# Kernel tuning notes

Hardware: AMD Instinct MI355X
Metric: run time of the kernel (lower is better)

Reference implementation:

```python
import jax, jax.numpy as jnp
import numpy as np

N_DOF = 7
HIDDEN = 256
BATCH = 32768
L_DIAG_OFFSET = 1e-3
FRICTION_EPS = 100.0


def setup_inputs() -> dict:
    key = jax.random.key(0)
    ks = jax.random.split(key, 16)
    n, H, B = N_DOF, HIDDEN, BATCH
    ntril = n * (n - 1) // 2

    def xavier(k, shape):
        fan_out, fan_in = shape
        std = (2.0 / (fan_in + fan_out)) ** 0.5
        return jax.random.normal(k, shape, jnp.float32) * std

    return {
        "q":   jax.random.normal(ks[0], (B, n), jnp.float32),
        "qd":  jax.random.normal(ks[1], (B, n), jnp.float32),
        "qdd": jax.random.normal(ks[2], (B, n), jnp.float32),
        # MLP trunk (hidden_depth = 3)
        "W0": xavier(ks[3], (H, n)),  "b0": jnp.zeros((H,), jnp.float32),
        "W1": xavier(ks[4], (H, H)),  "b1": jnp.zeros((H,), jnp.float32),
        "W2": xavier(ks[5], (H, H)),  "b2": jnp.zeros((H,), jnp.float32),
        # heads: gravity g, Cholesky diagonal, Cholesky strict-lower
        "Wg":  xavier(ks[6], (n, H)),     "bg":  jnp.zeros((n,), jnp.float32),
        "Wld": xavier(ks[7], (n, H)),     "bld": jnp.zeros((n,), jnp.float32),
        "Wlt": xavier(ks[8], (ntril, H)), "blt": jnp.zeros((ntril,), jnp.float32),
        # friction model parameters (init 0.1 each)
        "fd": jnp.full((n,), 0.1, jnp.float32),
        "fc": jnp.full((n,), 0.1, jnp.float32),
        "fs": jnp.full((n,), 0.1, jnp.float32),
        "fv": jnp.full((n,), 0.1, jnp.float32),
    }


def reference(q, qd, qdd, W0, b0, W1, b1, W2, b2, Wg, bg, Wld, bld, Wlt, blt,
              fd, fc, fs, fv):
    n = N_DOF
    B = q.shape[0]
    sp = jax.nn.softplus

    def net(qq):  # qq: [n] single sample
        h = sp(W0 @ qq + b0)
        h = sp(W1 @ h + b1)
        h = sp(W2 @ h + b2)
        g = Wg @ h + bg                      # [n]
        Ld_raw = Wld @ h + bld               # [n]
        Ld = sp(Ld_raw)                      # softplus diag activation
        Lt = Wlt @ h + blt                   # [n_tril]
        return (Ld, Lt), (g, Ld, Lt, Ld_raw)

    # per-sample Jacobians of (L_diag, L_tril) wrt q (forward mode, n_dof tangents)
    (jLd, jLt), (g, Ld, Lt, Ld_raw) = jax.vmap(jax.jacfwd(net, has_aux=True))(q)
    # jLd: [B,n,n], jLt: [B,ntril,n]

    idx = np.arange(n)
    rows, cols = np.tril_indices(n, -1)

    L = (jnp.zeros((B, n, n), q.dtype)
         .at[:, idx, idx].set(Ld)
         .at[:, rows, cols].set(Lt)
         + L_DIAG_OFFSET * jnp.eye(n, dtype=q.dtype))          # [B,n,n]
    L_dq = (jnp.zeros((B, n, n, n), q.dtype)
            .at[:, idx, idx, :].set(jLd)
            .at[:, rows, cols, :].set(jLt))                    # [B,n,n,n] (last = dq)

    LT = jnp.swapaxes(L, 1, 2)
    L_dqT = jnp.swapaxes(L_dq, 1, 2)

    Hm = jnp.einsum('bij,bjk->bik', L, LT)                      # mass matrix
    L_dt = jnp.einsum('bijc,bc->bij', L_dq, qd)                 # dL/dt
    L_dtT = jnp.swapaxes(L_dt, 1, 2)
    H_dt = jnp.einsum('bij,bjk->bik', L, L_dtT) + jnp.einsum('bij,bjk->bik', L_dt, LT)
    H_dq = (jnp.einsum('bijc,bjk->bikc', L_dq, LT)
            + jnp.einsum('bij,bjkc->bikc', L, L_dqT))           # [B,n,n,n]
    H_dq_qd = jnp.einsum('bijc,bj->bic', H_dq, qd)
    qdT_H_dq_qd = jnp.einsum('bi,bic->bc', qd, H_dq_qd)
    c = jnp.einsum('bij,bj->bi', H_dt, qd) - 0.5 * qdT_H_dq_qd  # Coriolis

    fv_c = jnp.clip(fv, 1e-3, None)
    tau_fric = (fc + fs * jnp.exp(-qd ** 2 / fv_c)) * jnp.tanh(FRICTION_EPS * qd) + fd * qd

    tau_pred = jnp.einsum('bij,bj->bi', Hm, qdd) + c + g + tau_fric
    return (tau_pred, Hm, c, g, tau_fric, Ld_raw)
```

## Files before the change

### kernel.cpp

```cpp
#include <hip/hip_runtime.h>
#include <cmath>

#define NDOF 7
#define HID  256
#define SPW  8
#define NCOL 64
#define SWZ(c) (((c) & 15) << 3)

typedef __bf16 bf16x8 __attribute__((ext_vector_type(8)));
typedef float  f32x4  __attribute__((ext_vector_type(4)));

#define OFF_W2 65536
#define OFF_WH 131072
#define OFF_W0 143360
#define WS_TOT 151552

__device__ __forceinline__ float softplus_fast(float x){
    float e = __expf(-fabsf(x));
    return fmaxf(x, 0.0f) + __logf(1.0f + e);
}
__device__ __forceinline__ float sigmoid_fast(float x){
    float e  = __expf(-fabsf(x));
    float rc = 1.0f / (1.0f + e);
    return (x >= 0.0f) ? rc : e * rc;
}
__device__ __forceinline__ float tanh_fast(float y){
    float e2 = __expf(-2.0f * fabsf(y));
    float t  = (1.0f - e2) / (1.0f + e2);
    return (y >= 0.0f) ? t : -t;
}
__device__ __forceinline__ unsigned bf16bits(float x){
    union { float f; unsigned u; } v; v.f = x;
    unsigned lsb = (v.u >> 16) & 1;
    return ((v.u + 0x7fffu + lsb) >> 16) & 0xffffu;
}

__global__ void convert_weights(const float* __restrict__ W1, const float* __restrict__ W2,
                                const float* __restrict__ Wg, const float* __restrict__ Wld,
                                const float* __restrict__ Wlt, const float* __restrict__ W0,
                                __bf16* __restrict__ ws)
{
    int i = blockIdx.x * 256 + threadIdx.x;
    if (i < OFF_W2)        ws[i] = (__bf16)W1[i];
    else if (i < OFF_WH)   ws[i] = (__bf16)W2[i - OFF_W2];
    else if (i < OFF_W0) {
        int j = i - OFF_WH;
        int r = j >> 8, k = j & 255;
        float v = 0.0f;
        if (r < 7)       v = Wg [r * HID + k];
        else if (r < 14) v = Wld[(r - 7) * HID + k];
        else if (r < 35) v = Wlt[(r - 14) * HID + k];
        ws[i] = (__bf16)v;
    } else if (i < WS_TOT) {
        int j = i - OFF_W0;
        int r = j >> 5, k = j & 31;
        ws[i] = (__bf16)((k < 7) ? W0[r * 7 + k] : 0.0f);
    }
}

template<int KK>
__device__ __forceinline__ void mlp_layer(
    const __bf16* __restrict__ Wb, int astride, const float* __restrict__ bp,
    __bf16* Xs, int w, int lo, int hi, const int* srcl, bool prim)
{
    f32x4 acc[4][4];
    #pragma unroll
    for (int mi = 0; mi < 4; ++mi)
        #pragma unroll
        for (int ni = 0; ni < 4; ++ni) acc[mi][ni] = (f32x4){0.f,0.f,0.f,0.f};

    #pragma unroll 2
    for (int kk = 0; kk < KK; ++kk){
        const int k0 = kk * 32 + hi * 8;
        bf16x8 a[4], bfr[4];
        #pragma unroll
        for (int mi = 0; mi < 4; ++mi)
            a[mi] = *reinterpret_cast<const bf16x8*>(Wb + (w * 64 + mi * 16 + lo) * astride + k0);
        #pragma unroll
        for (int ni = 0; ni < 4; ++ni){
            int col = ni * 16 + lo;
            bfr[ni] = *reinterpret_cast<const bf16x8*>(Xs + col * HID + (k0 ^ SWZ(col)));
        }
        __builtin_amdgcn_s_setprio(1);
        #pragma unroll
        for (int mi = 0; mi < 4; ++mi)
            #pragma unroll
            for (int ni = 0; ni < 4; ++ni)
                acc[mi][ni] = __builtin_amdgcn_mfma_f32_16x16x32_bf16(a[mi], bfr[ni], acc[mi][ni], 0, 0, 0);
        __builtin_amdgcn_s_setprio(0);
    }
    __syncthreads();

    #pragma unroll
    for (int mi = 0; mi < 4; ++mi){
        const int row0 = w * 64 + mi * 16 + hi * 4;
        float4 b4 = *reinterpret_cast<const float4*>(bp + row0);
        float h[4];
        unsigned pa, pb;
        {
            float sg[4];
            #pragma unroll
            for (int r = 0; r < 4; ++r){
                float z  = acc[mi][0][r] + ((const float*)&b4)[r];
                float e  = __expf(-fabsf(z));
                float rc = 1.0f / (1.0f + e);
                h[r]  = fmaxf(z, 0.0f) + __logf(1.0f + e);
                sg[r] = (z >= 0.0f) ? rc : e * rc;
            }
            pa = bf16bits(sg[0]) | (bf16bits(sg[1]) << 16);
            pb = bf16bits(sg[2]) | (bf16bits(sg[3]) << 16);
        }
        #pragma unroll
        for (int ni = 0; ni < 4; ++ni){
            int col = ni * 16 + lo;
            unsigned g01 = __shfl(pa, srcl[ni]);
            unsigned g23 = __shfl(pb, srcl[ni]);
            float sgf[4];
            { union { unsigned u; float f; } t;
              t.u = g01 << 16;          sgf[0] = t.f;
              t.u = g01 & 0xffff0000u;  sgf[1] = t.f;
              t.u = g23 << 16;          sgf[2] = t.f;
              t.u = g23 & 0xffff0000u;  sgf[3] = t.f; }
            union { uint2 u2; __bf16 b[4]; } pk;
            #pragma unroll
            for (int r = 0; r < 4; ++r){
                float v = (ni == 0 && prim) ? h[r] : sgf[r] * acc[mi][ni][r];
                pk.b[r] = (__bf16)v;
            }
            *reinterpret_cast<uint2*>(Xs + col * HID + ((row0 ^ SWZ(col)))) = pk.u2;
        }
    }
    __syncthreads();
}

__launch_bounds__(256, 4)
__global__ void dln_main(
    const float* __restrict__ q,  const float* __restrict__ qd, const float* __restrict__ qdd,
    const float* __restrict__ b0, const float* __restrict__ b1, const float* __restrict__ b2,
    const float* __restrict__ bg, const float* __restrict__ bld, const float* __restrict__ blt,
    const float* __restrict__ fd, const float* __restrict__ fc,
    const float* __restrict__ fs, const float* __restrict__ fv,
    const __bf16* __restrict__ wsb,
    float* __restrict__ out, int Btot)
{
    __shared__ __align__(16) unsigned char LDSB[32768];
    __bf16* Xs = (__bf16*)LDSB;

    const int tid = threadIdx.x;
    const int w   = tid >> 6;
    const int l   = tid & 63;
    const int lo  = l & 15;
    const int hi  = l >> 4;
    const int s0g = blockIdx.x * SPW;
    const bool prim = (lo < 8);

    int srcl[4];
    #pragma unroll
    for (int ni = 0; ni < 4; ++ni){
        int col  = ni * 16 + lo;
        int s    = (col < 8) ? col : (col - 8) / 7;
        srcl[ni] = (l & ~15) | s;
    }

    {
        uint4 z4 = {0,0,0,0};
        uint4* p = reinterpret_cast<uint4*>(LDSB + tid * 128);
        #pragma unroll
        for (int i = 0; i < 8; ++i) p[i] = z4;
    }
    __syncthreads();
    if (tid < 56){
        int s = tid / 7, d = tid - s * 7;
        Xs[s * HID + (d ^ SWZ(s))] = (__bf16)q[(s0g + s) * NDOF + d];
        int c = 8 + s * 7 + d;
        Xs[c * HID + (d ^ SWZ(c))] = (__bf16)1.0f;
    }
    __syncthreads();

    mlp_layer<1>(wsb + OFF_W0, 32,  b0, Xs, w, lo, hi, srcl, prim);
    mlp_layer<8>(wsb,          HID, b1, Xs, w, lo, hi, srcl, prim);
    mlp_layer<8>(wsb + OFF_W2, HID, b2, Xs, w, lo, hi, srcl, prim);

    f32x4 hacc[4];
    #pragma unroll
    for (int ni = 0; ni < 4; ++ni) hacc[ni] = (f32x4){0.f,0.f,0.f,0.f};
    if (w < 3){
        const __bf16* Wh = wsb + OFF_WH;
        #pragma unroll 2
        for (int kk = 0; kk < 8; ++kk){
            const int k0 = kk * 32 + hi * 8;
            bf16x8 a = *reinterpret_cast<const bf16x8*>(Wh + (w * 16 + lo) * HID + k0);
            __builtin_amdgcn_s_setprio(1);
            #pragma unroll
            for (int ni = 0; ni < 4; ++ni){
                int col = ni * 16 + lo;
                bf16x8 bfr = *reinterpret_cast<const bf16x8*>(Xs + col * HID + (k0 ^ SWZ(col)));
                hacc[ni] = __builtin_amdgcn_mfma_f32_16x16x32_bf16(a, bfr, hacc[ni], 0, 0, 0);
            }
            __builtin_amdgcn_s_setprio(0);
        }
    }
    __syncthreads();

    float* SCRT = (float*)LDSB;
    float* SGb  = (float*)(LDSB + 10496);
    float* UV   = (float*)(LDSB + 10752);
    float* LL   = (float*)(LDSB + 11264);

    if (w < 3){
        #pragma unroll
        for (int ni = 0; ni < 4; ++ni)
            #pragma unroll
            for (int r = 0; r < 4; ++r){
                int row = w * 16 + hi * 4 + r;
                if (row < 35) SCRT[(ni * 16 + lo) * 41 + row] = hacc[ni][r];
            }
    }
    __syncthreads();

    const bool t49 = (l < 49);
    const int  tt  = t49 ? l : 0;
    const int  r   = tt / 7;
    const int  c   = tt - r * 7;
    const int  B   = Btot;
    float* oH = out + (size_t)B * 7;
    float* oC = out + (size_t)B * 56;
    float* oG = out + (size_t)B * 63;
    float* oF = out + (size_t)B * 70;
    float* oL = out + (size_t)B * 77;

    for (int p = 0; p < 2; ++p){
        const int ss = p * 4 + w;
        const int Sg = __builtin_amdgcn_readfirstlane(s0g + ss);

        float qdv[7];
        #pragma unroll
        for (int d = 0; d < 7; ++d) qdv[d] = qd[Sg * 7 + d];
        const float qd_r  = qd [Sg * 7 + r];
        const float qd_c  = qd [Sg * 7 + c];
        const float qdd_c = qdd[Sg * 7 + c];

        const int colP  = ss * 41;
        const int tri_r = (r * (r - 1)) >> 1;

        float ldraw = SCRT[colP + 7 + r] + bld[r];
        float sg_r  = sigmoid_fast(ldraw);
        float Lrr   = softplus_fast(ldraw) + 1e-3f;
        float Lij   = 0.f;
        if (c < r)       Lij = SCRT[colP + 14 + tri_r + c] + blt[tri_r + c];
        else if (c == r) Lij = Lrr;

        if (t49)           LL[ss * 52 + tt] = Lij;
        if (t49 && r == c) SGb[ss * 8 + r]  = sg_r;

        float ux = qd_r * Lij;
        { float xs;
          xs = __shfl(ux, l + 7);  ux += (r + 1 <= 6) ? xs : 0.f;
          xs = __shfl(ux, l + 14); ux += (r + 2 <= 6) ? xs : 0.f;
          xs = __shfl(ux, l + 28); ux += (r + 4 <= 6) ? xs : 0.f; }
        if (t49 && r == 0) UV[ss * 16 + c] = ux;

        asm volatile("s_waitcnt lgkmcnt(0)" ::: "memory");
        __builtin_amdgcn_sched_barrier(0);

        float sgv[7];
        #pragma unroll
        for (int jj = 0; jj < 7; ++jj) sgv[jj] = SGb[ss * 8 + jj];

        const int colT = (8 + ss * 7 + c) * 41;
        float v = 0.f;
        #pragma unroll
        for (int jj = 0; jj < 7; ++jj){
            constexpr int triT[7] = {0,0,1,3,6,10,15};
            int   row = (jj == r) ? (7 + jj) : (14 + triT[jj] + r);
            float x   = SCRT[colT + row];
            float val = (jj == r) ? sgv[jj] * x : ((jj > r) ? x : 0.f);
            v = fmaf(qdv[jj], val, v);
        }

        {
            int   rowF   = (r == c) ? (7 + r) : (14 + tri_r + c);
            float scaleF = (r == c) ? sg_r : ((r > c) ? 1.f : 0.f);
            float acc2 = 0.f;
            #pragma unroll
            for (int cc = 0; cc < 7; ++cc)
                acc2 = fmaf(qdv[cc], SCRT[(8 + ss * 7 + cc) * 41 + rowF], acc2);
            float ldt = acc2 * scaleF;

            float wx = v * qd_c;
            { float xs;
              xs = __shfl(wx, l + 1); wx += (c + 1 <= 6) ? xs : 0.f;
              xs = __shfl(wx, l + 2); wx += (c + 2 <= 6) ? xs : 0.f;
              xs = __shfl(wx, l + 4); wx += (c + 4 <= 6) ? xs : 0.f; }
            if (t49 && c == 0) UV[ss * 16 + 8 + r] = wx;

            asm volatile("s_waitcnt lgkmcnt(0)" ::: "memory");
            __builtin_amdgcn_sched_barrier(0);

            float u_c  = UV[ss * 16 + c];
            float u_r  = UV[ss * 16 + r];
            float w2_c = UV[ss * 16 + 8 + c];

            float qx = u_r * v;
            { float xs;
              xs = __shfl(qx, l + 7);  qx += (r + 1 <= 6) ? xs : 0.f;
              xs = __shfl(qx, l + 14); qx += (r + 2 <= 6) ? xs : 0.f;
              xs = __shfl(qx, l + 28); qx += (r + 4 <= 6) ? xs : 0.f; }

            float cx = Lij * w2_c + ldt * u_c;
            { float xs;
              xs = __shfl(cx, l + 1); cx += (c + 1 <= 6) ? xs : 0.f;
              xs = __shfl(cx, l + 2); cx += (c + 2 <= 6) ? xs : 0.f;
              xs = __shfl(cx, l + 4); cx += (c + 4 <= 6) ? xs : 0.f; }

            float hm = 0.f;
            #pragma unroll
            for (int k = 0; k < 7; ++k)
                hm = fmaf(LL[ss * 52 + r * 7 + k], LL[ss * 52 + c * 7 + k], hm);

            float tx = hm * qdd_c;
            { float xs;
              xs = __shfl(tx, l + 1); tx += (c + 1 <= 6) ? xs : 0.f;
              xs = __shfl(tx, l + 2); tx += (c + 2 <= 6) ? xs : 0.f;
              xs = __shfl(tx, l + 4); tx += (c + 4 <= 6) ? xs : 0.f; }

            float qh_r = __shfl(qx, r);
            float gv   = SCRT[colP + r] + bg[r];
            float fvc  = fmaxf(fv[r], 1e-3f);
            float tf   = (fc[r] + fs[r] * __expf(-qd_r * qd_r / fvc)) * tanh_fast(100.0f * qd_r) + fd[r] * qd_r;
            float cfin = cx - qh_r;
            float tau  = cfin + gv + tf + tx;

            if (t49) oH[(size_t)Sg * 49 + tt] = hm;
            if (t49 && c == 0){
                out[Sg * 7 + r] = tau;
                oC[Sg * 7 + r]  = cfin;
                oG[Sg * 7 + r]  = gv;
                oF[Sg * 7 + r]  = tf;
                oL[Sg * 7 + r]  = ldraw;
            }
        }
    }
}

extern "C" void kernel_launch(void* const* d_in, const int* in_sizes, int n_in,
                              void* d_out, int out_size, void* d_ws, size_t ws_size,
                              hipStream_t stream) {
    const float* q   = (const float*)d_in[0];
    const float* qd  = (const float*)d_in[1];
    const float* qdd = (const float*)d_in[2];
    const float* W0  = (const float*)d_in[3];
    const float* b0  = (const float*)d_in[4];
    const float* W1  = (const float*)d_in[5];
    const float* b1  = (const float*)d_in[6];
    const float* W2  = (const float*)d_in[7];
    const float* b2  = (const float*)d_in[8];
    const float* Wg  = (const float*)d_in[9];
    const float* bg  = (const float*)d_in[10];
    const float* Wld = (const float*)d_in[11];
    const float* bld = (const float*)d_in[12];
    const float* Wlt = (const float*)d_in[13];
    const float* blt = (const float*)d_in[14];
    const float* fd  = (const float*)d_in[15];
    const float* fc  = (const float*)d_in[16];
    const float* fs  = (const float*)d_in[17];
    const float* fv  = (const float*)d_in[18];

    const int Btot = in_sizes[0] / NDOF;
    __bf16* wsb = (__bf16*)d_ws;

    convert_weights<<<dim3(WS_TOT / 256), dim3(256), 0, stream>>>(W1, W2, Wg, Wld, Wlt, W0, wsb);
    dln_main<<<dim3(Btot / SPW), dim3(256), 0, stream>>>(q, qd, qdd, b0, b1, b2,
                                                         bg, bld, blt,
                                                         fd, fc, fs, fv,
                                                         wsb, (float*)d_out, Btot);
}
```

Baseline: 269.7 us.

## Split MLP layer N-dimension into halves to cut registers and raise occupancy

Each MLP layer now computes its 64 sample-columns in two halves of 32, holding 8 accumulator tiles per wave instead of 16. Occupancy is raised by moving launch bounds from 4 to 5 blocks. Reads and writes of each half touch disjoint columns, so the trailing barrier per layer is dropped and one barrier is added after the trunk. The change also narrows the LDS swizzle, zeroes only the first 64 elements of each column, removes s_setprio hints and disables K-loop unrolling. In exchange, the weight A-fragments are loaded twice per layer, and bank-conflict behaviour changes with the new swizzle.

```diff
diff --git a/kernel.cpp b/kernel.cpp
--- a/kernel.cpp
+++ b/kernel.cpp
@@ -5,7 +5,7 @@
 #define HID  256
 #define SPW  8
 #define NCOL 64
-#define SWZ(c) (((c) & 15) << 3)
+#define SWZ(c) (((c) & 7) << 3)
 
 typedef __bf16 bf16x8 __attribute__((ext_vector_type(8)));
 typedef float  f32x4  __attribute__((ext_vector_type(4)));
@@ -63,77 +63,79 @@
     const __bf16* __restrict__ Wb, int astride, const float* __restrict__ bp,
     __bf16* Xs, int w, int lo, int hi, const int* srcl, bool prim)
 {
-    f32x4 acc[4][4];
+    unsigned pa[4], pb[4];
+    float    h[4][4];
+
     #pragma unroll
-    for (int mi = 0; mi < 4; ++mi)
-        #pragma unroll
-        for (int ni = 0; ni < 4; ++ni) acc[mi][ni] = (f32x4){0.f,0.f,0.f,0.f};
-
-    #pragma unroll 2
-    for (int kk = 0; kk < KK; ++kk){
-        const int k0 = kk * 32 + hi * 8;
-        bf16x8 a[4], bfr[4];
+    for (int nh = 0; nh < 2; ++nh){
+        f32x4 acc[4][2];
         #pragma unroll
         for (int mi = 0; mi < 4; ++mi)
-            a[mi] = *reinterpret_cast<const bf16x8*>(Wb + (w * 64 + mi * 16 + lo) * astride + k0);
-        #pragma unroll
-        for (int ni = 0; ni < 4; ++ni){
-            int col = ni * 16 + lo;
-            bfr[ni] = *reinterpret_cast<const bf16x8*>(Xs + col * HID + (k0 ^ SWZ(col)));
-        }
-        __builtin_amdgcn_s_setprio(1);
-        #pragma unroll
-        for (int mi = 0; mi < 4; ++mi)
-            #pragma unroll
-            for (int ni = 0; ni < 4; ++ni)
-                acc[mi][ni] = __builtin_amdgcn_mfma_f32_16x16x32_bf16(a[mi], bfr[ni], acc[mi][ni], 0, 0, 0);
-        __builtin_amdgcn_s_setprio(0);
-    }
-    __syncthreads();
-
-    #pragma unroll
-    for (int mi = 0; mi < 4; ++mi){
-        const int row0 = w * 64 + mi * 16 + hi * 4;
-        float4 b4 = *reinterpret_cast<const float4*>(bp + row0);
-        float h[4];
-        unsigned pa, pb;
-        {
-            float sg[4];
-            #pragma unroll
-            for (int r = 0; r < 4; ++r){
-                float z  = acc[mi][0][r] + ((const float*)&b4)[r];
-                float e  = __expf(-fabsf(z));
-                float rc = 1.0f / (1.0f + e);
-                h[r]  = fmaxf(z, 0.0f) + __logf(1.0f + e);
-                sg[r] = (z >= 0.0f) ? rc : e * rc;
-            }
-            pa = bf16bits(sg[0]) | (bf16bits(sg[1]) << 16);
-            pb = bf16bits(sg[2]) | (bf16bits(sg[3]) << 16);
-        }
-        #pragma unroll
-        for (int ni = 0; ni < 4; ++ni){
-            int col = ni * 16 + lo;
-            unsigned g01 = __shfl(pa, srcl[ni]);
-            unsigned g23 = __shfl(pb, srcl[ni]);
-            float sgf[4];
-            { union { unsigned u; float f; } t;
-              t.u = g01 << 16;          sgf[0] = t.f;
-              t.u = g01 & 0xffff0000u;  sgf[1] = t.f;
-              t.u = g23 << 16;          sgf[2] = t.f;
-              t.u = g23 & 0xffff0000u;  sgf[3] = t.f; }
-            union { uint2 u2; __bf16 b[4]; } pk;
-            #pragma unroll
-            for (int r = 0; r < 4; ++r){
-                float v = (ni == 0 && prim) ? h[r] : sgf[r] * acc[mi][ni][r];
-                pk.b[r] = (__bf16)v;
-            }
-            *reinterpret_cast<uint2*>(Xs + col * HID + ((row0 ^ SWZ(col)))) = pk.u2;
-        }
-    }
-    __syncthreads();
-}
-
-__launch_bounds__(256, 4)
+            #pragma unroll
+            for (int j = 0; j < 2; ++j) acc[mi][j] = (f32x4){0.f,0.f,0.f,0.f};
+
+        #pragma unroll 1
+        for (int kk = 0; kk < KK; ++kk){
+            const int k0 = kk * 32 + hi * 8;
+            bf16x8 a[4], bfr[2];
+            #pragma unroll
+            for (int mi = 0; mi < 4; ++mi)
+                a[mi] = *reinterpret_cast<const bf16x8*>(Wb + (w * 64 + mi * 16 + lo) * astride + k0);
+            #pragma unroll
+            for (int j = 0; j < 2; ++j){
+                int col = (nh * 2 + j) * 16 + lo;
+                bfr[j] = *reinterpret_cast<const bf16x8*>(Xs + col * HID + (k0 ^ SWZ(col)));
+            }
+            #pragma unroll
+            for (int mi = 0; mi < 4; ++mi)
+                #pragma unroll
+                for (int j = 0; j < 2; ++j)
+                    acc[mi][j] = __builtin_amdgcn_mfma_f32_16x16x32_bf16(a[mi], bfr[j], acc[mi][j], 0, 0, 0);
+        }
+        __syncthreads();
+
+        #pragma unroll
+        for (int mi = 0; mi < 4; ++mi){
+            const int row0 = w * 64 + mi * 16 + hi * 4;
+            if (nh == 0){
+                float4 b4 = *reinterpret_cast<const float4*>(bp + row0);
+                float sg[4];
+                #pragma unroll
+                for (int r = 0; r < 4; ++r){
+                    float z  = acc[mi][0][r] + ((const float*)&b4)[r];
+                    float e  = __expf(-fabsf(z));
+                    float rc = 1.0f / (1.0f + e);
+                    h[mi][r] = fmaxf(z, 0.0f) + __logf(1.0f + e);
+                    sg[r] = (z >= 0.0f) ? rc : e * rc;
+                }
+                pa[mi] = bf16bits(sg[0]) | (bf16bits(sg[1]) << 16);
+                pb[mi] = bf16bits(sg[2]) | (bf16bits(sg[3]) << 16);
+            }
+            #pragma unroll
+            for (int j = 0; j < 2; ++j){
+                const int ni  = nh * 2 + j;
+                const int col = ni * 16 + lo;
+                unsigned g01 = __shfl(pa[mi], srcl[ni]);
+                unsigned g23 = __shfl(pb[mi], srcl[ni]);
+                float sgf[4];
+                { union { unsigned u; float f; } t;
+                  t.u = g01 << 16;          sgf[0] = t.f;
+                  t.u = g01 & 0xffff0000u;  sgf[1] = t.f;
+                  t.u = g23 << 16;          sgf[2] = t.f;
+                  t.u = g23 & 0xffff0000u;  sgf[3] = t.f; }
+                union { uint2 u2; __bf16 b[4]; } pk;
+                #pragma unroll
+                for (int r = 0; r < 4; ++r){
+                    float v = (ni == 0 && prim) ? h[mi][r] : sgf[r] * acc[mi][j][r];
+                    pk.b[r] = (__bf16)v;
+                }
+                *reinterpret_cast<uint2*>(Xs + col * HID + (row0 ^ SWZ(col))) = pk.u2;
+            }
+        }
+    }
+}
+
+__launch_bounds__(256, 5)
 __global__ void dln_main(
     const float* __restrict__ q,  const float* __restrict__ qd, const float* __restrict__ qdd,
     const float* __restrict__ b0, const float* __restrict__ b1, const float* __restrict__ b2,
@@ -163,10 +165,10 @@
     }
 
     {
+        int col = tid >> 2, part = tid & 3;
         uint4 z4 = {0,0,0,0};
-        uint4* p = reinterpret_cast<uint4*>(LDSB + tid * 128);
-        #pragma unroll
-        for (int i = 0; i < 8; ++i) p[i] = z4;
+        *reinterpret_cast<uint4*>(Xs + col * HID + part * 16)     = z4;
+        *reinterpret_cast<uint4*>(Xs + col * HID + part * 16 + 8) = z4;
     }
     __syncthreads();
     if (tid < 56){
@@ -180,6 +182,7 @@
     mlp_layer<1>(wsb + OFF_W0, 32,  b0, Xs, w, lo, hi, srcl, prim);
     mlp_layer<8>(wsb,          HID, b1, Xs, w, lo, hi, srcl, prim);
     mlp_layer<8>(wsb + OFF_W2, HID, b2, Xs, w, lo, hi, srcl, prim);
+    __syncthreads();
 
     f32x4 hacc[4];
     #pragma unroll
@@ -190,14 +193,12 @@
         for (int kk = 0; kk < 8; ++kk){
             const int k0 = kk * 32 + hi * 8;
             bf16x8 a = *reinterpret_cast<const bf16x8*>(Wh + (w * 16 + lo) * HID + k0);
-            __builtin_amdgcn_s_setprio(1);
             #pragma unroll
             for (int ni = 0; ni < 4; ++ni){
                 int col = ni * 16 + lo;
                 bf16x8 bfr = *reinterpret_cast<const bf16x8*>(Xs + col * HID + (k0 ^ SWZ(col)));
                 hacc[ni] = __builtin_amdgcn_mfma_f32_16x16x32_bf16(a, bfr, hacc[ni], 0, 0, 0);
             }
-            __builtin_amdgcn_s_setprio(0);
         }
     }
     __syncthreads();
```

Result: slower. 358.5 us (+33.0%).
